# Optimization experiments

Hardware: AMD Instinct MI355X
Metric: run time of the kernel (lower is better)

Reference implementation:

```python
import jax, jax.numpy as jnp
import numpy as np

N, C, V, T = 256, 256, 25, 20
K = 3            # kernel_size
PAD = 1          # padding
O = 256          # out_channels
C4 = C // 4
EPS = 1e-5


def _bn(x, p, axes_shape):
    # p: (4, dim) = gamma, beta, running_mean, running_var (eval-mode BN)
    g, b, m, v = (p[i].reshape(axes_shape) for i in range(4))
    return (x - m) * (g / jnp.sqrt(v + EPS)) + b


def setup_inputs() -> dict:
    key = jax.random.key(0)
    ks = jax.random.split(key, 12)
    rn = lambda k, s, sc=0.05: jax.random.normal(k, s, jnp.float32) * sc
    bn = lambda k, d: jnp.stack([
        1.0 + 0.1 * jax.random.normal(jax.random.fold_in(k, 0), (d,), jnp.float32),  # gamma
        0.1 * jax.random.normal(jax.random.fold_in(k, 1), (d,), jnp.float32),        # beta
        0.1 * jax.random.normal(jax.random.fold_in(k, 2), (d,), jnp.float32),        # mean
        0.5 + jax.random.uniform(jax.random.fold_in(k, 3), (d,), jnp.float32),       # var
    ])
    return {
        "x": jax.random.normal(ks[0], (N, C, V, T), jnp.float32),
        "Wg1": rn(ks[1], (2 * T, T), 0.2),      # Linear T -> 2T (no bias)
        "Wg2": rn(ks[2], (K, 2 * T), 0.2),      # Linear 2T -> K (no bias)
        "Wl1": rn(ks[3], (C4, C, K)),           # Conv1d C -> C/4, kernel K
        "Wl2": rn(ks[4], (C, C4)),              # Conv1d C/4 -> C, kernel 1
        "Wc2": rn(ks[5], (O, C)),               # 1x1 Conv2d C -> O (no bias)
        "bng": bn(ks[6], 2 * T),
        "bnl": bn(ks[7], C4),
        "bn1p": bn(ks[8], C),
        "bn2p": bn(ks[9], O),
    }


def reference(x, Wg1, Wg2, Wl1, Wl2, Wc2, bng, bnl, bn1p, bn2p):
    n, c, v, t = x.shape
    new_x = jnp.transpose(x, (0, 1, 3, 2))            # (N, C, T, V)
    pooled = new_x.mean(axis=-1)                       # (N, C, T)  adaptive_avg_pool over V

    # --- G branch: per-(n,c) dynamic temporal kernel ---
    h = pooled.reshape(n * c, t) @ Wg1.T               # (NC, 2T)
    h = jax.nn.relu(_bn(h, bng, (1, 2 * t)))
    kern = jax.nn.softmax(h @ Wg2.T, axis=-1)          # (NC, K)
    kern = kern.reshape(n, c, K)

    # --- L branch: local temporal excitation ---
    l = jax.lax.conv_general_dilated(
        pooled, Wl1, window_strides=(1,), padding=[(K // 2, K // 2)],
        dimension_numbers=("NCH", "OIH", "NCH"))      # (N, C4, T)
    l = jax.nn.relu(_bn(l, bnl, (1, C4, 1)))
    l = jax.nn.sigmoid(jnp.einsum("oc,nct->not", Wl2, l))  # (N, C, T)
    new_x = new_x + l[..., None]                       # (N, C, T, V)

    # --- dynamic depthwise temporal conv (groups = N*C) ---
    padded = jnp.pad(new_x, ((0, 0), (0, 0), (PAD, PAD), (0, 0)))
    out = sum(kern[:, :, k, None, None] * padded[:, :, k:k + t, :] for k in range(K))

    out = jnp.transpose(out, (0, 1, 3, 2))             # (N, C, V, T)
    out = jax.nn.relu(_bn(out, bn1p, (1, c, 1, 1)))    # bn1 + relu; dropout in eval = identity
    out = jnp.einsum("oc,ncvt->novt", Wc2, out)        # 1x1 conv
    out = jax.nn.relu(_bn(out, bn2p, (1, O, 1, 1)))    # bn2 + relu
    return out
```

## Files before the change

kernel.cpp:

```cpp
#include <hip/hip_runtime.h>
#include <hip/hip_bf16.h>
#include <math.h>

#define N_ 256
#define C_ 256
#define V_ 25
#define T_ 20
#define C4_ 64
#define O_ 256
#define VT_ 500
#define EPS_ 1e-5f

typedef unsigned short ushort_t;
typedef unsigned short us4 __attribute__((ext_vector_type(4)));
typedef short short8 __attribute__((ext_vector_type(8)));
typedef float f32x4 __attribute__((ext_vector_type(4)));

__device__ __forceinline__ float bf2f(ushort_t u) {
    unsigned int v = ((unsigned int)u) << 16;
    return __builtin_bit_cast(float, v);
}
__device__ __forceinline__ ushort_t f2bf(float f) {
    unsigned int u = __builtin_bit_cast(unsigned int, f);
    unsigned int r = u + 0x7fffu + ((u >> 16) & 1u);
    return (ushort_t)(r >> 16);
}

__device__ __forceinline__ void bar_lds() {
    __builtin_amdgcn_sched_barrier(0);
    asm volatile("s_waitcnt lgkmcnt(0)" ::: "memory");
    __builtin_amdgcn_s_barrier();
    __builtin_amdgcn_sched_barrier(0);
}

__global__ __launch_bounds__(256) void k_pool(const float* __restrict__ x,
                                              float* __restrict__ pooled,
                                              const float* __restrict__ Wc2,
                                              ushort_t* __restrict__ wbf,
                                              const float* __restrict__ Wl1,
                                              ushort_t* __restrict__ awl,
                                              const float* __restrict__ Wl2,
                                              ushort_t* __restrict__ wl2bf) {
    int tid = threadIdx.x;
    if (blockIdx.x >= 8272) {
        int o = (blockIdx.x - 8272) * 256 + tid;
        int c4 = o / 768;
        int rem = o - c4 * 768;
        int k = rem >> 8, c = rem & 255;
        awl[o] = f2bf(Wl1[(c4 * 256 + c) * 3 + k]);
        return;
    }
    if (blockIdx.x >= 8256) {
        int i = (blockIdx.x - 8256) * 256 + tid;
        f32x4 v = ((const f32x4*)Wl2)[i];
        us4 o; o.x = f2bf(v.x); o.y = f2bf(v.y); o.z = f2bf(v.z); o.w = f2bf(v.w);
        ((us4*)wl2bf)[i] = o;
        return;
    }
    if (blockIdx.x >= 8192) {
        int i = (blockIdx.x - 8192) * 256 + tid;
        f32x4 v = ((const f32x4*)Wc2)[i];
        us4 o; o.x = f2bf(v.x); o.y = f2bf(v.y); o.z = f2bf(v.z); o.w = f2bf(v.w);
        ((us4*)wbf)[i] = o;
        return;
    }
    __shared__ float xs[8][504];
    const f32x4* src = (const f32x4*)(x + (size_t)blockIdx.x * 8 * VT_);
    for (int i = tid; i < 1000; i += 256) {
        int r = i / 125, cidx = (i % 125) * 4;
        *(f32x4*)&xs[r][cidx] = src[i];
    }
    __syncthreads();
    if (tid < 160) {
        int r = tid / 20, t = tid % 20;
        float s = 0.f;
#pragma unroll
        for (int v = 0; v < V_; ++v) s += xs[r][v * T_ + t];
        pooled[blockIdx.x * 160 + tid] = s * 0.04f;
    }
}

__global__ __launch_bounds__(256) void k_gl(const float* __restrict__ pooled,
                                            const float* __restrict__ Wg1,
                                            const float* __restrict__ Wg2,
                                            const float* __restrict__ bng,
                                            const float* __restrict__ bnl,
                                            const ushort_t* __restrict__ awl,
                                            const ushort_t* __restrict__ wl2bf,
                                            float* __restrict__ kern,
                                            float* __restrict__ l2out) {
    __shared__ __align__(16) char smem[76288];
    float (*pp)[22] = (float (*)[22])smem;
    float* sl = (float*)(smem + 22528);
    float* bl = (float*)(smem + 22528 + 256);
    char* lsT = smem + 23040;
    char* bpt = smem + 27136;

    int tid = threadIdx.x;
    int n = blockIdx.x;

    {
        const f32x4* pn = (const f32x4*)(pooled + n * (C_ * T_));
#pragma unroll
        for (int q = 0; q < 5; ++q) {
            int id = q * 256 + tid;
            int c = id / 5, qq = id % 5;
            f32x4 v = pn[id];
            pp[c][qq * 4 + 0] = v.x; pp[c][qq * 4 + 1] = v.y;
            pp[c][qq * 4 + 2] = v.z; pp[c][qq * 4 + 3] = v.w;
        }
    }
    if (tid < C4_) {
        float g = bnl[tid], b = bnl[64 + tid];
        float m = bnl[128 + tid], v = bnl[192 + tid];
        float s = g * rsqrtf(v + EPS_);
        sl[tid] = s; bl[tid] = b - m * s;
    }
    {
        unsigned int* z = (unsigned int*)lsT;
        for (int i = tid; i < 384; i += 256) z[640 + i] = 0u;
    }
    __syncthreads();

    float p[20];
#pragma unroll
    for (int t = 0; t < 20; ++t) p[t] = pp[tid][t];

    {
        float l0 = 0.f, l1 = 0.f, l2 = 0.f;
#pragma unroll 4
        for (int j = 0; j < 40; ++j) {
            float h = 0.f;
#pragma unroll
            for (int t = 0; t < 20; ++t) h = fmaf(Wg1[j * 20 + t], p[t], h);
            float g = bng[j], b = bng[40 + j];
            float m = bng[80 + j], v = bng[120 + j];
            float s = g * rsqrtf(v + EPS_);
            h = fmaxf(fmaf(h, s, b - m * s), 0.f);
            l0 = fmaf(Wg2[j], h, l0);
            l1 = fmaf(Wg2[40 + j], h, l1);
            l2 = fmaf(Wg2[80 + j], h, l2);
        }
        float mx = fmaxf(l0, fmaxf(l1, l2));
        float e0 = __expf(l0 - mx), e1 = __expf(l1 - mx), e2 = __expf(l2 - mx);
        float inv = 1.f / (e0 + e1 + e2);
        float* kp = kern + (n * C_ + tid) * 3;
        kp[0] = e0 * inv; kp[1] = e1 * inv; kp[2] = e2 * inv;
    }

    {
        int c = tid;
#pragma unroll
        for (int k = 0; k < 3; ++k) {
            int col2base = (k * 256 + c) * 2;
#pragma unroll
            for (int t = 0; t < 20; ++t) {
                int i = t + k - 1;
                float v = (i >= 0 && i < 20) ? p[i] : 0.f;
                int byte = t * 1536 + (col2base ^ ((t & 7) << 4));
                *(ushort_t*)(bpt + byte) = f2bf(v);
            }
        }
    }
    __syncthreads();

    int lane = tid & 63, wave = tid >> 6;
    int mrow = lane & 15, kof = (lane >> 4) * 8, prow = (lane >> 4) * 4;

    {
        f32x4 acc0 = (f32x4){0.f, 0.f, 0.f, 0.f};
        f32x4 acc1 = (f32x4){0.f, 0.f, 0.f, 0.f};
        int swz = ((mrow & 7) << 4);
#pragma unroll 4
        for (int kk = 0; kk < 768; kk += 32) {
            short8 af = *(const short8*)(awl + (wave * 16 + mrow) * 768 + kk + kof);
            short8 b0 = *(const short8*)(bpt + mrow * 1536 + (((kk + kof) * 2) ^ swz));
            short8 b1 = *(const short8*)(bpt + (16 + mrow) * 1536 + (((kk + kof) * 2) ^ swz));
            acc0 = __builtin_amdgcn_mfma_f32_16x16x32_bf16(af, b0, acc0, 0, 0, 0);
            acc1 = __builtin_amdgcn_mfma_f32_16x16x32_bf16(af, b1, acc1, 0, 0, 0);
        }
        f32x4 sv = *(const f32x4*)(sl + wave * 16 + prow);
        f32x4 bv = *(const f32x4*)(bl + wave * 16 + prow);
#pragma unroll
        for (int nt = 0; nt < 2; ++nt) {
            int t = nt * 16 + (lane & 15);
            if (t < 20) {
                f32x4 a = nt ? acc1 : acc0;
#pragma unroll
                for (int r = 0; r < 4; ++r) {
                    int c4 = wave * 16 + prow + r;
                    float v = fmaxf(fmaf(a[r], sv[r], bv[r]), 0.f);
                    int byte = t * 128 + ((c4 * 2) ^ ((t & 7) << 4));
                    *(ushort_t*)(lsT + byte) = f2bf(v);
                }
            }
        }
    }
    __syncthreads();

    {
        f32x4 acc[4][2];
#pragma unroll
        for (int mtl = 0; mtl < 4; ++mtl)
#pragma unroll
            for (int nt = 0; nt < 2; ++nt) acc[mtl][nt] = (f32x4){0.f, 0.f, 0.f, 0.f};
        int swz = ((mrow & 7) << 4);
#pragma unroll
        for (int kk = 0; kk < 64; kk += 32) {
            short8 af[4], bfr[2];
#pragma unroll
            for (int mtl = 0; mtl < 4; ++mtl)
                af[mtl] = *(const short8*)(wl2bf + (wave * 64 + mtl * 16 + mrow) * 64 + kk + kof);
#pragma unroll
            for (int nt = 0; nt < 2; ++nt)
                bfr[nt] = *(const short8*)(lsT + (nt * 16 + mrow) * 128 + (((kk + kof) * 2) ^ swz));
#pragma unroll
            for (int mtl = 0; mtl < 4; ++mtl)
#pragma unroll
                for (int nt = 0; nt < 2; ++nt)
                    acc[mtl][nt] = __builtin_amdgcn_mfma_f32_16x16x32_bf16(af[mtl], bfr[nt], acc[mtl][nt], 0, 0, 0);
        }
#pragma unroll
        for (int nt = 0; nt < 2; ++nt) {
            int t = nt * 16 + (lane & 15);
            if (t < 20) {
#pragma unroll
                for (int mtl = 0; mtl < 4; ++mtl) {
#pragma unroll
                    for (int r = 0; r < 4; ++r) {
                        int c = wave * 64 + mtl * 16 + prow + r;
                        float v = acc[mtl][nt][r];
                        l2out[(n * C_ + c) * T_ + t] = 1.f / (1.f + __expf(-v));
                    }
                }
            }
        }
    }
}

#define YSTRIDE 264
#define YBUF 26400

__global__ __launch_bounds__(512, 2) void k_main(const float* __restrict__ x,
                                                 const ushort_t* __restrict__ wbf,
                                                 const float* __restrict__ bn1p,
                                                 const float* __restrict__ bn2p,
                                                 const float* __restrict__ kern,
                                                 const float* __restrict__ l2g,
                                                 float* __restrict__ out) {
    __shared__ __align__(16) ushort_t yTs[2 * YBUF];

    int tid = threadIdx.x;
    int n = blockIdx.x;
    const float* xn = x + (size_t)n * (C_ * V_ * T_);
    int lane = tid & 63;
    int wave = tid >> 6;
    int mrow = lane & 15;
    int kof = (lane >> 4) * 8;
    int prow = (lane >> 4) * 4;
    int obase = wave * 32;

    float s1, b1, k0, k1, k2, l2r[20];
    {
        int c = tid & 255;
        float g1 = bn1p[c], be1 = bn1p[256 + c];
        float m1 = bn1p[512 + c], v1 = bn1p[768 + c];
        s1 = g1 * rsqrtf(v1 + EPS_);
        b1 = be1 - m1 * s1;
        const float* kp = kern + (n * C_ + c) * 3;
        k0 = kp[0]; k1 = kp[1]; k2 = kp[2];
        const f32x4* lp = (const f32x4*)(l2g + (n * C_ + c) * T_);
#pragma unroll
        for (int q = 0; q < 5; ++q) {
            f32x4 v = lp[q];
            l2r[q*4+0] = v.x; l2r[q*4+1] = v.y; l2r[q*4+2] = v.z; l2r[q*4+3] = v.w;
        }
    }
    float s2, b2;
    {
        int c2 = obase + (lane & 31);
        float g2 = bn2p[c2], be2 = bn2p[256 + c2];
        float m2 = bn2p[512 + c2], v2 = bn2p[768 + c2];
        s2 = g2 * rsqrtf(v2 + EPS_);
        b2 = be2 - m2 * s2;
    }

    short8 afr[2][8];
#pragma unroll
    for (int mt = 0; mt < 2; ++mt)
#pragma unroll
        for (int k8 = 0; k8 < 8; ++k8)
            afr[mt][k8] = *(const short8*)(wbf + (obase + mt * 16 + mrow) * C_ + k8 * 32 + kof);

    int off[13];
#pragma unroll
    for (int q = 0; q < 12; ++q) {
        int id = q * 512 + tid;
        off[q] = (id / 25) * VT_ + (id % 25) * 4;
    }
    off[12] = ((6144 + tid) / 25) * VT_ + ((6144 + tid) % 25) * 4;

    const int ctb[7] = {0, 16, 32, 48, 64, 80, 84};

    f32x4 ld[13];
#pragma unroll
    for (int q = 0; q < 12; ++q) ld[q] = *(const f32x4*)(xn + off[q]);
    if (tid < 256) ld[12] = *(const f32x4*)(xn + off[12]);

    {
        ushort_t* xs = yTs;
#pragma unroll
        for (int q = 0; q < 12; ++q) {
            int id = q * 512 + tid;
            us4 o; o.x = f2bf(ld[q].x); o.y = f2bf(ld[q].y);
            o.z = f2bf(ld[q].z); o.w = f2bf(ld[q].w);
            *(us4*)(xs + (id / 25) * 100 + (id % 25) * 4) = o;
        }
        if (tid < 256) {
            int id = 6144 + tid;
            us4 o; o.x = f2bf(ld[12].x); o.y = f2bf(ld[12].y);
            o.z = f2bf(ld[12].z); o.w = f2bf(ld[12].w);
            *(us4*)(xs + (id / 25) * 100 + (id % 25) * 4) = o;
        }
    }
    bar_lds();
    float yv[3][20];
    {
        const ushort_t* xs = yTs;
        int c = tid & 255;
#pragma unroll
        for (int r3 = 0; r3 < 3; ++r3) {
            int v = (r3 < 2) ? (r3 * 2 + (tid >> 8)) : 4;
            if (r3 < 2 || tid < 256) {
                float a[22];
                a[0] = 0.f; a[21] = 0.f;
#pragma unroll
                for (int qq = 0; qq < 5; ++qq) {
                    us4 u = *(const us4*)(xs + c * 100 + v * 20 + qq * 4);
                    a[qq*4 + 1] = bf2f(u.x) + l2r[qq*4 + 0];
                    a[qq*4 + 2] = bf2f(u.y) + l2r[qq*4 + 1];
                    a[qq*4 + 3] = bf2f(u.z) + l2r[qq*4 + 2];
                    a[qq*4 + 4] = bf2f(u.w) + l2r[qq*4 + 3];
                }
#pragma unroll
                for (int t = 0; t < 20; ++t) {
                    float z = fmaf(k0, a[t], fmaf(k1, a[t + 1], k2 * a[t + 2]));
                    yv[r3][t] = fmaxf(fmaf(z, s1, b1), 0.f);
                }
            }
        }
    }
    bar_lds();
    {
        ushort_t* yb = yTs;
        int c = tid & 255;
#pragma unroll
        for (int r3 = 0; r3 < 3; ++r3) {
            int v = (r3 < 2) ? (r3 * 2 + (tid >> 8)) : 4;
            if (r3 < 2 || tid < 256) {
#pragma unroll
                for (int t = 0; t < 20; ++t)
                    yb[(v * 20 + t) * YSTRIDE + c] = f2bf(yv[r3][t]);
            }
        }
    }
    bar_lds();

    int buf = 0;
    float* outn0 = out + (size_t)n * (O_ * VT_);

#pragma unroll 1
    for (int tile = 0; tile < 5; ++tile) {
        if (tile < 4) {
#pragma unroll
            for (int q = 0; q < 12; ++q)
                ld[q] = *(const f32x4*)(xn + off[q] + (tile + 1) * 100);
            if (tid < 256) ld[12] = *(const f32x4*)(xn + off[12] + (tile + 1) * 100);
        }
        __builtin_amdgcn_sched_barrier(0);

        {
            const ushort_t* yb = yTs + buf * YBUF;
            f32x4 acc[2][7];
#pragma unroll
            for (int mt = 0; mt < 2; ++mt)
#pragma unroll
                for (int j = 0; j < 7; ++j) acc[mt][j] = (f32x4){0.f, 0.f, 0.f, 0.f};
#pragma unroll
            for (int k8 = 0; k8 < 8; ++k8) {
#pragma unroll
                for (int ct = 0; ct < 7; ++ct) {
                    short8 b = *(const short8*)(yb + (ctb[ct] + mrow) * YSTRIDE + k8 * 32 + kof);
                    acc[0][ct] = __builtin_amdgcn_mfma_f32_16x16x32_bf16(afr[0][k8], b, acc[0][ct], 0, 0, 0);
                    acc[1][ct] = __builtin_amdgcn_mfma_f32_16x16x32_bf16(afr[1][k8], b, acc[1][ct], 0, 0, 0);
                }
            }
#pragma unroll
            for (int mt = 0; mt < 2; ++mt) {
#pragma unroll
                for (int r = 0; r < 4; ++r) {
                    int lsrc = mt * 16 + prow + r;
                    float s2w = __shfl(s2, lsrc);
                    float b2w = __shfl(b2, lsrc);
                    float* orow = outn0 + (size_t)(obase + lsrc) * VT_ + tile * 100;
#pragma unroll
                    for (int j = 0; j < 7; ++j) {
                        if (!(j == 6 && mrow < 12)) {
                            orow[ctb[j] + mrow] =
                                fmaxf(fmaf(acc[mt][j][r], s2w, b2w), 0.f);
                        }
                    }
                }
            }
        }

        if (tile < 4) {
            ushort_t* xs = yTs + (buf ^ 1) * YBUF;
#pragma unroll
            for (int q = 0; q < 12; ++q) {
                int id = q * 512 + tid;
                us4 o; o.x = f2bf(ld[q].x); o.y = f2bf(ld[q].y);
                o.z = f2bf(ld[q].z); o.w = f2bf(ld[q].w);
                *(us4*)(xs + (id / 25) * 100 + (id % 25) * 4) = o;
            }
            if (tid < 256) {
                int id = 6144 + tid;
                us4 o; o.x = f2bf(ld[12].x); o.y = f2bf(ld[12].y);
                o.z = f2bf(ld[12].z); o.w = f2bf(ld[12].w);
                *(us4*)(xs + (id / 25) * 100 + (id % 25) * 4) = o;
            }
        }
        bar_lds();

        if (tile < 4) {
            const ushort_t* xs = yTs + (buf ^ 1) * YBUF;
            int c = tid & 255;
#pragma unroll
            for (int r3 = 0; r3 < 3; ++r3) {
                int v = (r3 < 2) ? (r3 * 2 + (tid >> 8)) : 4;
                if (r3 < 2 || tid < 256) {
                    float a[22];
                    a[0] = 0.f; a[21] = 0.f;
#pragma unroll
                    for (int qq = 0; qq < 5; ++qq) {
                        us4 u = *(const us4*)(xs + c * 100 + v * 20 + qq * 4);
                        a[qq*4 + 1] = bf2f(u.x) + l2r[qq*4 + 0];
                        a[qq*4 + 2] = bf2f(u.y) + l2r[qq*4 + 1];
                        a[qq*4 + 3] = bf2f(u.z) + l2r[qq*4 + 2];
                        a[qq*4 + 4] = bf2f(u.w) + l2r[qq*4 + 3];
                    }
#pragma unroll
                    for (int t = 0; t < 20; ++t) {
                        float z = fmaf(k0, a[t], fmaf(k1, a[t + 1], k2 * a[t + 2]));
                        yv[r3][t] = fmaxf(fmaf(z, s1, b1), 0.f);
                    }
                }
            }
        }
        bar_lds();

        if (tile < 4) {
            ushort_t* yb = yTs + (buf ^ 1) * YBUF;
            int c = tid & 255;
#pragma unroll
            for (int r3 = 0; r3 < 3; ++r3) {
                int v = (r3 < 2) ? (r3 * 2 + (tid >> 8)) : 4;
                if (r3 < 2 || tid < 256) {
#pragma unroll
                    for (int t = 0; t < 20; ++t)
                        yb[(v * 20 + t) * YSTRIDE + c] = f2bf(yv[r3][t]);
                }
            }
        }
        bar_lds();
        buf ^= 1;
    }
}

extern "C" void kernel_launch(void* const* d_in, const int* in_sizes, int n_in,
                              void* d_out, int out_size, void* d_ws, size_t ws_size,
                              hipStream_t stream) {
    const float* x   = (const float*)d_in[0];
    const float* Wg1 = (const float*)d_in[1];
    const float* Wg2 = (const float*)d_in[2];
    const float* Wl1 = (const float*)d_in[3];
    const float* Wl2 = (const float*)d_in[4];
    const float* Wc2 = (const float*)d_in[5];
    const float* bng = (const float*)d_in[6];
    const float* bnl = (const float*)d_in[7];
    const float* bn1p = (const float*)d_in[8];
    const float* bn2p = (const float*)d_in[9];
    float* out = (float*)d_out;

    float* ws = (float*)d_ws;
    float* pooled = ws;
    float* kern   = ws + 1310720;
    float* l2g    = ws + 1310720 + 196608;
    ushort_t* wbf   = (ushort_t*)(ws + 2818048);
    ushort_t* wl2bf = (ushort_t*)(ws + 2818048 + 32768);
    ushort_t* awl   = (ushort_t*)(ws + 2818048 + 40960);

    k_pool<<<dim3(8464), dim3(256), 0, stream>>>(x, pooled, Wc2, wbf, Wl1, awl, Wl2, wl2bf);
    k_gl<<<dim3(N_), dim3(256), 0, stream>>>(pooled, Wg1, Wg2, bng, bnl, awl, wl2bf, kern, l2g);
    k_main<<<dim3(N_), dim3(512), 0, stream>>>(x, wbf, bn1p, bn2p, kern, l2g, out);
}
```

Measured before the change: 418.1 us.

## Give x staging its own LDS buffer and prefetch input two tiles ahead

Shared memory is split into a dedicated bf16 staging buffer for x plus a double-buffered y buffer, 156800 bytes in total. Each thread's temporal conv now writes its bf16 result straight into the next y buffer instead of holding it in registers across an extra barrier. This drops one block barrier per tile and lets global loads run two tiles ahead of use. The larger LDS footprint forces one block per CU, and launch bounds are lowered to match, trading occupancy for less synchronisation and deeper load overlap.

```diff
diff --git a/kernel.cpp b/kernel.cpp
--- a/kernel.cpp
+++ b/kernel.cpp
@@ -241,20 +241,23 @@
 #define YSTRIDE 264
 #define YBUF 26400
 
-__global__ __launch_bounds__(512, 2) void k_main(const float* __restrict__ x,
+__global__ __launch_bounds__(512, 1) void k_main(const float* __restrict__ x,
                                                  const ushort_t* __restrict__ wbf,
                                                  const float* __restrict__ bn1p,
                                                  const float* __restrict__ bn2p,
                                                  const float* __restrict__ kern,
                                                  const float* __restrict__ l2g,
                                                  float* __restrict__ out) {
-    __shared__ __align__(16) ushort_t yTs[2 * YBUF];
+    __shared__ __align__(16) char smem[156800];
+    ushort_t* xs = (ushort_t*)smem;
 
     int tid = threadIdx.x;
     int n = blockIdx.x;
     const float* xn = x + (size_t)n * (C_ * V_ * T_);
     int lane = tid & 63;
     int wave = tid >> 6;
+    int half = tid >> 8;
+    int cc = tid & 255;
     int mrow = lane & 15;
     int kof = (lane >> 4) * 8;
     int prow = (lane >> 4) * 4;
@@ -262,14 +265,13 @@
 
     float s1, b1, k0, k1, k2, l2r[20];
     {
-        int c = tid & 255;
-        float g1 = bn1p[c], be1 = bn1p[256 + c];
-        float m1 = bn1p[512 + c], v1 = bn1p[768 + c];
+        float g1 = bn1p[cc], be1 = bn1p[256 + cc];
+        float m1 = bn1p[512 + cc], v1 = bn1p[768 + cc];
         s1 = g1 * rsqrtf(v1 + EPS_);
         b1 = be1 - m1 * s1;
-        const float* kp = kern + (n * C_ + c) * 3;
+        const float* kp = kern + (n * C_ + cc) * 3;
         k0 = kp[0]; k1 = kp[1]; k2 = kp[2];
-        const f32x4* lp = (const f32x4*)(l2g + (n * C_ + c) * T_);
+        const f32x4* lp = (const f32x4*)(l2g + (n * C_ + cc) * T_);
 #pragma unroll
         for (int q = 0; q < 5; ++q) {
             f32x4 v = lp[q];
@@ -302,68 +304,66 @@
 
     const int ctb[7] = {0, 16, 32, 48, 64, 80, 84};
 
+#define ISSUE_LD(TILE)                                                        \
+    {                                                                         \
+        _Pragma("unroll")                                                     \
+        for (int q = 0; q < 12; ++q)                                          \
+            ld[q] = *(const f32x4*)(xn + off[q] + (TILE) * 100);              \
+        if (half == 0) ld[12] = *(const f32x4*)(xn + off[12] + (TILE) * 100); \
+    }
+
+#define WRITE_XS()                                                            \
+    {                                                                         \
+        _Pragma("unroll")                                                     \
+        for (int q = 0; q < 12; ++q) {                                        \
+            int id = q * 512 + tid;                                           \
+            us4 o; o.x = f2bf(ld[q].x); o.y = f2bf(ld[q].y);                  \
+            o.z = f2bf(ld[q].z); o.w = f2bf(ld[q].w);                         \
+            *(us4*)(xs + (id / 25) * 100 + (id % 25) * 4) = o;                \
+        }                                                                     \
+        if (half == 0) {                                                      \
+            int id = 6144 + tid;                                              \
+            us4 o; o.x = f2bf(ld[12].x); o.y = f2bf(ld[12].y);                \
+            o.z = f2bf(ld[12].z); o.w = f2bf(ld[12].w);                       \
+            *(us4*)(xs + (id / 25) * 100 + (id % 25) * 4) = o;                \
+        }                                                                     \
+    }
+
+#define CONV_TO(YB)                                                           \
+    {                                                                         \
+        ushort_t* yb_ = (YB);                                                 \
+        _Pragma("unroll")                                                     \
+        for (int r3 = 0; r3 < 3; ++r3) {                                      \
+            int v = (r3 < 2) ? (r3 * 2 + half) : 4;                           \
+            if (r3 < 2 || half == 0) {                                        \
+                float a[22];                                                  \
+                a[0] = 0.f; a[21] = 0.f;                                      \
+                _Pragma("unroll")                                             \
+                for (int qq = 0; qq < 5; ++qq) {                              \
+                    us4 u = *(const us4*)(xs + cc * 100 + v * 20 + qq * 4);   \
+                    a[qq*4 + 1] = bf2f(u.x) + l2r[qq*4 + 0];                  \
+                    a[qq*4 + 2] = bf2f(u.y) + l2r[qq*4 + 1];                  \
+                    a[qq*4 + 3] = bf2f(u.z) + l2r[qq*4 + 2];                  \
+                    a[qq*4 + 4] = bf2f(u.w) + l2r[qq*4 + 3];                  \
+                }                                                             \
+                _Pragma("unroll")                                             \
+                for (int t = 0; t < 20; ++t) {                                \
+                    float z = fmaf(k0, a[t], fmaf(k1, a[t + 1], k2 * a[t + 2]));\
+                    yb_[(v * 20 + t) * YSTRIDE + cc] =                        \
+                        f2bf(fmaxf(fmaf(z, s1, b1), 0.f));                    \
+                }                                                             \
+            }                                                                 \
+        }                                                                     \
+    }
+
     f32x4 ld[13];
-#pragma unroll
-    for (int q = 0; q < 12; ++q) ld[q] = *(const f32x4*)(xn + off[q]);
-    if (tid < 256) ld[12] = *(const f32x4*)(xn + off[12]);
-
-    {
-        ushort_t* xs = yTs;
-#pragma unroll
-        for (int q = 0; q < 12; ++q) {
-            int id = q * 512 + tid;
-            us4 o; o.x = f2bf(ld[q].x); o.y = f2bf(ld[q].y);
-            o.z = f2bf(ld[q].z); o.w = f2bf(ld[q].w);
-            *(us4*)(xs + (id / 25) * 100 + (id % 25) * 4) = o;
-        }
-        if (tid < 256) {
-            int id = 6144 + tid;
-            us4 o; o.x = f2bf(ld[12].x); o.y = f2bf(ld[12].y);
-            o.z = f2bf(ld[12].z); o.w = f2bf(ld[12].w);
-            *(us4*)(xs + (id / 25) * 100 + (id % 25) * 4) = o;
-        }
-    }
+    ISSUE_LD(0);
+    WRITE_XS();
     bar_lds();
-    float yv[3][20];
-    {
-        const ushort_t* xs = yTs;
-        int c = tid & 255;
-#pragma unroll
-        for (int r3 = 0; r3 < 3; ++r3) {
-            int v = (r3 < 2) ? (r3 * 2 + (tid >> 8)) : 4;
-            if (r3 < 2 || tid < 256) {
-                float a[22];
-                a[0] = 0.f; a[21] = 0.f;
-#pragma unroll
-                for (int qq = 0; qq < 5; ++qq) {
-                    us4 u = *(const us4*)(xs + c * 100 + v * 20 + qq * 4);
-                    a[qq*4 + 1] = bf2f(u.x) + l2r[qq*4 + 0];
-                    a[qq*4 + 2] = bf2f(u.y) + l2r[qq*4 + 1];
-                    a[qq*4 + 3] = bf2f(u.z) + l2r[qq*4 + 2];
-                    a[qq*4 + 4] = bf2f(u.w) + l2r[qq*4 + 3];
-                }
-#pragma unroll
-                for (int t = 0; t < 20; ++t) {
-                    float z = fmaf(k0, a[t], fmaf(k1, a[t + 1], k2 * a[t + 2]));
-                    yv[r3][t] = fmaxf(fmaf(z, s1, b1), 0.f);
-                }
-            }
-        }
-    }
+    ISSUE_LD(1);
+    CONV_TO((ushort_t*)(smem + 51200));
     bar_lds();
-    {
-        ushort_t* yb = yTs;
-        int c = tid & 255;
-#pragma unroll
-        for (int r3 = 0; r3 < 3; ++r3) {
-            int v = (r3 < 2) ? (r3 * 2 + (tid >> 8)) : 4;
-            if (r3 < 2 || tid < 256) {
-#pragma unroll
-                for (int t = 0; t < 20; ++t)
-                    yb[(v * 20 + t) * YSTRIDE + c] = f2bf(yv[r3][t]);
-            }
-        }
-    }
+    WRITE_XS();
     bar_lds();
 
     int buf = 0;
@@ -371,16 +371,11 @@
 
 #pragma unroll 1
     for (int tile = 0; tile < 5; ++tile) {
-        if (tile < 4) {
-#pragma unroll
-            for (int q = 0; q < 12; ++q)
-                ld[q] = *(const f32x4*)(xn + off[q] + (tile + 1) * 100);
-            if (tid < 256) ld[12] = *(const f32x4*)(xn + off[12] + (tile + 1) * 100);
-        }
+        if (tile < 3) ISSUE_LD(tile + 2);
         __builtin_amdgcn_sched_barrier(0);
 
         {
-            const ushort_t* yb = yTs + buf * YBUF;
+            const ushort_t* yb = (const ushort_t*)(smem + 51200) + buf * YBUF;
             f32x4 acc[2][7];
 #pragma unroll
             for (int mt = 0; mt < 2; ++mt)
@@ -415,66 +410,16 @@
         }
 
         if (tile < 4) {
-            ushort_t* xs = yTs + (buf ^ 1) * YBUF;
-#pragma unroll
-            for (int q = 0; q < 12; ++q) {
-                int id = q * 512 + tid;
-                us4 o; o.x = f2bf(ld[q].x); o.y = f2bf(ld[q].y);
-                o.z = f2bf(ld[q].z); o.w = f2bf(ld[q].w);
-                *(us4*)(xs + (id / 25) * 100 + (id % 25) * 4) = o;
-            }
-            if (tid < 256) {
-                int id = 6144 + tid;
-                us4 o; o.x = f2bf(ld[12].x); o.y = f2bf(ld[12].y);
-                o.z = f2bf(ld[12].z); o.w = f2bf(ld[12].w);
-                *(us4*)(xs + (id / 25) * 100 + (id % 25) * 4) = o;
-            }
-        }
-        bar_lds();
-
-        if (tile < 4) {
-            const ushort_t* xs = yTs + (buf ^ 1) * YBUF;
-            int c = tid & 255;
-#pragma unroll
-            for (int r3 = 0; r3 < 3; ++r3) {
-                int v = (r3 < 2) ? (r3 * 2 + (tid >> 8)) : 4;
-                if (r3 < 2 || tid < 256) {
-                    float a[22];
-                    a[0] = 0.f; a[21] = 0.f;
-#pragma unroll
-                    for (int qq = 0; qq < 5; ++qq) {
-                        us4 u = *(const us4*)(xs + c * 100 + v * 20 + qq * 4);
-                        a[qq*4 + 1] = bf2f(u.x) + l2r[qq*4 + 0];
-                        a[qq*4 + 2] = bf2f(u.y) + l2r[qq*4 + 1];
-                        a[qq*4 + 3] = bf2f(u.z) + l2r[qq*4 + 2];
-                        a[qq*4 + 4] = bf2f(u.w) + l2r[qq*4 + 3];
-                    }
-#pragma unroll
-                    for (int t = 0; t < 20; ++t) {
-                        float z = fmaf(k0, a[t], fmaf(k1, a[t + 1], k2 * a[t + 2]));
-                        yv[r3][t] = fmaxf(fmaf(z, s1, b1), 0.f);
-                    }
-                }
-            }
-        }
-        bar_lds();
-
-        if (tile < 4) {
-            ushort_t* yb = yTs + (buf ^ 1) * YBUF;
-            int c = tid & 255;
-#pragma unroll
-            for (int r3 = 0; r3 < 3; ++r3) {
-                int v = (r3 < 2) ? (r3 * 2 + (tid >> 8)) : 4;
-                if (r3 < 2 || tid < 256) {
-#pragma unroll
-                    for (int t = 0; t < 20; ++t)
-                        yb[(v * 20 + t) * YSTRIDE + c] = f2bf(yv[r3][t]);
-                }
-            }
-        }
-        bar_lds();
+            CONV_TO((ushort_t*)(smem + 51200) + (buf ^ 1) * YBUF);
+            bar_lds();
+            if (tile < 3) WRITE_XS();
+            bar_lds();
+        }
         buf ^= 1;
     }
+#undef ISSUE_LD
+#undef WRITE_XS
+#undef CONV_TO
 }
 
 extern "C" void kernel_launch(void* const* d_in, const int* in_sizes, int n_in,
```

Result: faster. 378.0 us (-9.6%).
